# Kernel optimization log

Hardware: AMD Instinct MI355X
Metric: run time of the kernel (lower is better)

## Reference

```python
import jax, jax.numpy as jnp
import numpy as np

B, T, D_IN, D_OUT = 4, 2048, 1024, 1024


def setup_inputs() -> dict:
    key = jax.random.key(0)
    k1, k2, k3, k4 = jax.random.split(key, 4)
    s = 0.02  # keep activations in a sane range
    x = jax.random.normal(k1, (B, T, D_IN), dtype=jnp.float32)
    Wq = jax.random.normal(k2, (D_IN, D_OUT), dtype=jnp.float32) * s
    Wk = jax.random.normal(k3, (D_IN, D_OUT), dtype=jnp.float32) * s
    Wv = jax.random.normal(k4, (D_IN, D_OUT), dtype=jnp.float32) * s
    return {"x": x, "Wq": Wq, "Wk": Wk, "Wv": Wv}


def reference(x, Wq, Wk, Wv):
    # Linear projections (torch Linear: y = x @ W^T, here W stored as [d_in, d_out])
    q = jnp.einsum('btd,de->bte', x, Wq)
    k = jnp.einsum('btd,de,->bte', x, Wk, jnp.float32(1.0)) if False else jnp.einsum('btd,de->bte', x, Wk)
    v = jnp.einsum('btd,de->bte', x, Wv)
    # Full [B, T, T] score matrix (faithful to the hand-rolled implementation)
    scores = jnp.einsum('bqe,bke->bqk', q, k)
    T_ = x.shape[1]
    causal = jnp.triu(jnp.ones((T_, T_), dtype=bool), k=1)  # True above diagonal
    scores = jnp.where(causal[None, :, :], -jnp.inf, scores)
    scale = 1.0 / jnp.sqrt(jnp.asarray(k.shape[-1], dtype=scores.dtype))
    attn = jax.nn.softmax(scores * scale, axis=-1)
    # dropout p=0.0 -> identity
    return jnp.einsum('bqk,bke->bqe', attn, v)
```

## Files before the change

### kernel.cpp

```cpp
#include <hip/hip_runtime.h>
#include <hip/hip_bf16.h>
#include <cstdint>

typedef __attribute__((ext_vector_type(8))) short short8;
typedef __attribute__((ext_vector_type(4))) short short4v;
typedef __attribute__((ext_vector_type(4))) float floatx4;
typedef unsigned short ushort;

__device__ __forceinline__ float bf2f(ushort u) {
  unsigned int x = ((unsigned int)u) << 16;
  return __builtin_bit_cast(float, x);
}
__device__ __forceinline__ ushort f2bf(float f) {
  unsigned int x = __builtin_bit_cast(unsigned int, f);
  x += 0x7fffu + ((x >> 16) & 1u);
  return (ushort)(x >> 16);
}

__device__ __forceinline__ void gload_lds16(const void* g, void* l) {
  __builtin_amdgcn_global_load_lds(
      (const __attribute__((address_space(1))) void*)g,
      (__attribute__((address_space(3))) void*)l, 16, 0, 0);
}


__global__ __launch_bounds__(256) void cvtx_kernel(const float* __restrict__ x,
                                                   ushort* __restrict__ xb) {
  int i = blockIdx.x * 256 + threadIdx.x;
  const float4* xf = (const float4*)x;
  float4 a = xf[i * 2], b = xf[i * 2 + 1];
  short8 o;
  o[0] = (short)f2bf(a.x); o[1] = (short)f2bf(a.y);
  o[2] = (short)f2bf(a.z); o[3] = (short)f2bf(a.w);
  o[4] = (short)f2bf(b.x); o[5] = (short)f2bf(b.y);
  o[6] = (short)f2bf(b.z); o[7] = (short)f2bf(b.w);
  ((short8*)xb)[i] = o;
}

__global__ __launch_bounds__(256) void wt_kernel(const float* __restrict__ Wq,
                                                 const float* __restrict__ Wk,
                                                 const float* __restrict__ Wv,
                                                 ushort* __restrict__ Wt) {
  int z = blockIdx.z;
  const float* W = z == 0 ? Wq : (z == 1 ? Wk : Wv);
  ushort* O = Wt + (size_t)z * 1024 * 1024;
  __shared__ float tile[64][65];
  int c0 = blockIdx.x * 64;
  int r0 = blockIdx.y * 64;
  int tid = threadIdx.x;
#pragma unroll
  for (int i = 0; i < 4; ++i) {
    int c = tid + i * 256; int rr = c >> 4, q = c & 15;
    float4 v = *(const float4*)&W[(size_t)(r0 + rr) * 1024 + c0 + q * 4];
    tile[rr][q * 4 + 0] = v.x; tile[rr][q * 4 + 1] = v.y;
    tile[rr][q * 4 + 2] = v.z; tile[rr][q * 4 + 3] = v.w;
  }
  __syncthreads();
#pragma unroll
  for (int i = 0; i < 2; ++i) {
    int c = tid + i * 256; int oc = c >> 3, q = c & 7;
    short8 o;
#pragma unroll
    for (int j = 0; j < 8; ++j) o[j] = (short)f2bf(tile[q * 8 + j][oc]);
    *(short8*)&O[(size_t)(c0 + oc) * 1024 + r0 + q * 8] = o;
  }
}


__global__ __launch_bounds__(256, 2) void qkv2_kernel(const ushort* __restrict__ A,
                                                      const ushort* __restrict__ Bm,
                                                      ushort* __restrict__ Qo,
                                                      ushort* __restrict__ Ko,
                                                      ushort* __restrict__ Vt) {
  __shared__ __align__(16) ushort ldsA[3][128 * 32];
  __shared__ __align__(16) ushort ldsB[3][256 * 32];

  const int tid = threadIdx.x;
  const int lane = tid & 63;
  const int wave = tid >> 6;
  const int r15 = lane & 15;
  const int kg = lane >> 4;

  int orig = blockIdx.y * 64 + blockIdx.x;
  int swz = (orig & 7) * 96 + (orig >> 3);
  int bx = swz / 12;
  int by = swz % 12;
  const int m0 = bx * 128;
  const int n0 = by * 256;

  const ushort* Ag = A + (size_t)m0 * 1024;
  const ushort* Bg = Bm + (size_t)n0 * 1024;

  const int NKT = 32;

  floatx4 acc[8][4] = {};

  auto stage = [&](int kt, int slot) {
    int k0 = kt * 32;
#pragma unroll
    for (int i = 0; i < 2; ++i) {
      int c = tid + i * 256;
      int d = c * 16;
      int L = d ^ (((d >> 7) & 3) << 4);
      gload_lds16(Ag + (size_t)(L >> 6) * 1024 + k0 + ((L & 63) >> 1),
                  &ldsA[slot][c * 8]);
    }
#pragma unroll
    for (int i = 0; i < 4; ++i) {
      int c = tid + i * 256;
      int d = c * 16;
      int L = d ^ (((d >> 7) & 3) << 4);
      gload_lds16(Bg + (size_t)(L >> 6) * 1024 + k0 + ((L & 63) >> 1),
                  &ldsB[slot][c * 8]);
    }
  };

  auto ldA = [&](int slot, int m) -> short8 {
    int row = m * 16 + r15;
    int P = (row * 64 + kg * 16) ^ (((row >> 1) & 3) << 4);
    return *(const short8*)((const char*)&ldsA[slot][0] + P);
  };
  auto ldB = [&](int slot, int n) -> short8 {
    int row = wave * 64 + n * 16 + r15;
    int P = (row * 64 + kg * 16) ^ (((row >> 1) & 3) << 4);
    return *(const short8*)((const char*)&ldsB[slot][0] + P);
  };

  stage(0, 0);
  stage(1, 1);
  asm volatile("s_waitcnt vmcnt(6)" ::: "memory");
  __builtin_amdgcn_s_barrier();

  int cur = 0;
  for (int kt = 0; kt < NKT; ++kt) {
    short8 bfrag[4], afrag[4];
#pragma unroll
    for (int n = 0; n < 4; ++n) bfrag[n] = ldB(cur, n);
#pragma unroll
    for (int m = 0; m < 4; ++m) afrag[m] = ldA(cur, m);
    if (kt + 2 < NKT) {
      int slot = cur + 2; if (slot >= 3) slot -= 3;
      stage(kt + 2, slot);
    }
    __builtin_amdgcn_s_barrier();
    asm volatile("s_waitcnt lgkmcnt(0)" ::: "memory");
    __builtin_amdgcn_sched_barrier(0);
    __builtin_amdgcn_s_setprio(1);
#pragma unroll
    for (int m = 0; m < 4; ++m)
#pragma unroll
      for (int n = 0; n < 4; ++n)
        acc[m][n] = __builtin_amdgcn_mfma_f32_16x16x32_bf16(afrag[m], bfrag[n], acc[m][n], 0, 0, 0);
    __builtin_amdgcn_s_setprio(0);
    __builtin_amdgcn_s_barrier();

#pragma unroll
    for (int m = 0; m < 4; ++m) afrag[m] = ldA(cur, m + 4);
    if (kt >= NKT - 3) {
      asm volatile("s_waitcnt vmcnt(0)" ::: "memory");
    } else {
      asm volatile("s_waitcnt vmcnt(6)" ::: "memory");
    }
    __builtin_amdgcn_s_barrier();
    asm volatile("s_waitcnt lgkmcnt(0)" ::: "memory");
    __builtin_amdgcn_sched_barrier(0);
    __builtin_amdgcn_s_setprio(1);
#pragma unroll
    for (int m = 0; m < 4; ++m)
#pragma unroll
      for (int n = 0; n < 4; ++n)
        acc[m + 4][n] = __builtin_amdgcn_mfma_f32_16x16x32_bf16(afrag[m], bfrag[n], acc[m + 4][n], 0, 0, 0);
    __builtin_amdgcn_s_setprio(0);
    __builtin_amdgcn_s_barrier();

    ++cur; if (cur >= 3) cur = 0;
  }

  const int z = n0 >> 10;
  const int rq = kg * 4;
  if (z < 2) {
    ushort* Cz = z == 0 ? Qo : Ko;
    const int cb = n0 & 1023;
#pragma unroll
    for (int m = 0; m < 8; ++m) {
#pragma unroll
      for (int n = 0; n < 4; ++n) {
        int gc = cb + wave * 64 + n * 16 + r15;
#pragma unroll
        for (int r = 0; r < 4; ++r) {
          int gr = m0 + m * 16 + rq + r;
          Cz[(size_t)gr * 1024 + gc] = f2bf(acc[m][n][r]);
        }
      }
    }
  } else {
#pragma unroll
    for (int m = 0; m < 8; ++m) {
      int gr = m0 + m * 16 + rq;
      int b = gr >> 11;
      int t = gr & 2047;
      ushort* Vb = Vt + (size_t)b * 1024 * 2048;
#pragma unroll
      for (int n = 0; n < 4; ++n) {
        int e = (n0 - 2048) + wave * 64 + n * 16 + r15;
        short4v o;
#pragma unroll
        for (int r = 0; r < 4; ++r) o[r] = (short)f2bf(acc[m][n][r]);
        *(short4v*)&Vb[(size_t)e * 2048 + t] = o;
      }
    }
  }
}


template <bool OUT_BF16>
__device__ __forceinline__ void gemm_tn_core(const ushort* __restrict__ A,
                                             const ushort* __restrict__ B,
                                             void* __restrict__ C,
                                             int lda, int ldb, int ldc,
                                             int m0, int n0, int kTiles) {
  __shared__ __align__(16) ushort Asm[2][128 * 32];
  __shared__ __align__(16) ushort Bsm[2][128 * 32];
  const int tid = threadIdx.x;
  const int lane = tid & 63;
  const int wave = tid >> 6;
  const int wrow = (wave >> 1) * 64;
  const int wcol = (wave & 1) * 64;
  const int r15 = lane & 15;
  const int kg = (lane >> 4) * 8;

  floatx4 acc[4][4] = {};

  const ushort* Ag = A + (size_t)m0 * lda;
  const ushort* Bg = B + (size_t)n0 * ldb;

  auto stage = [&](int buf, int kt) {
    int k0 = kt * 32;
#pragma unroll
    for (int i = 0; i < 2; ++i) {
      int c = tid + i * 256;
      gload_lds16(Ag + (size_t)(c >> 2) * lda + k0 + (c & 3) * 8, &Asm[buf][c * 8]);
    }
#pragma unroll
    for (int i = 0; i < 2; ++i) {
      int c = tid + i * 256;
      gload_lds16(Bg + (size_t)(c >> 2) * ldb + k0 + (c & 3) * 8, &Bsm[buf][c * 8]);
    }
  };

  stage(0, 0);
  for (int kt = 0; kt < kTiles; ++kt) {
    int cur = kt & 1;
    __syncthreads();
    if (kt + 1 < kTiles) stage(cur ^ 1, kt + 1);
    const ushort* As = Asm[cur];
    const ushort* Bs = Bsm[cur];
    short8 af[4], bfr[4];
#pragma unroll
    for (int m = 0; m < 4; ++m)
      af[m] = *(const short8*)&As[(wrow + m * 16 + r15) * 32 + kg];
#pragma unroll
    for (int n = 0; n < 4; ++n)
      bfr[n] = *(const short8*)&Bs[(wcol + n * 16 + r15) * 32 + kg];
#pragma unroll
    for (int m = 0; m < 4; ++m)
#pragma unroll
      for (int n = 0; n < 4; ++n)
        acc[m][n] = __builtin_amdgcn_mfma_f32_16x16x32_bf16(af[m], bfr[n], acc[m][n], 0, 0, 0);
  }

  const int rq = (lane >> 4) * 4;
#pragma unroll
  for (int m = 0; m < 4; ++m) {
#pragma unroll
    for (int n = 0; n < 4; ++n) {
      int gc = n0 + wcol + n * 16 + r15;
#pragma unroll
      for (int r = 0; r < 4; ++r) {
        int gr = m0 + wrow + m * 16 + rq + r;
        if (OUT_BF16)
          ((ushort*)C)[(size_t)gr * ldc + gc] = f2bf(acc[m][n][r]);
        else
          ((float*)C)[(size_t)gr * ldc + gc] = acc[m][n][r];
      }
    }
  }
}

__global__ __launch_bounds__(256) void s_kernel(const ushort* __restrict__ Q,
                                                const ushort* __restrict__ K,
                                                ushort* __restrict__ S) {
  int t = blockIdx.x;
  int qb = (int)((sqrtf(8.f * (float)t + 1.f) - 1.f) * 0.5f);
  while ((qb + 1) * (qb + 2) / 2 <= t) ++qb;
  while (qb * (qb + 1) / 2 > t) --qb;
  int kb = t - qb * (qb + 1) / 2;
  size_t b = blockIdx.y;
  gemm_tn_core<true>(Q + b * 2048 * 1024, K + b * 2048 * 1024, S + b * 2048 * 2048,
                     1024, 1024, 2048, qb * 128, kb * 128, 32);
}

__global__ __launch_bounds__(256) void pv_kernel(const ushort* __restrict__ P,
                                                 const ushort* __restrict__ Vt,
                                                 float* __restrict__ O) {
  int qb = blockIdx.x;
  size_t b = blockIdx.z;
  gemm_tn_core<false>(P + b * 2048 * 2048, Vt + b * 1024 * 2048, O + b * 2048 * 1024,
                      2048, 2048, 1024, qb * 128, blockIdx.y * 128, (qb + 1) * 4);
}

__global__ __launch_bounds__(256) void softmax_kernel(ushort* __restrict__ S) {
  const int r = blockIdx.x;
  const int b = blockIdx.y;
  ushort* row = S + ((size_t)b * 2048 + r) * 2048;
  const int len = r + 1;
  const int padEnd = ((r >> 7) + 1) << 7;
  const int tid = threadIdx.x;
  const int base = tid * 8;
  const float scale = 0.03125f;

  float v[8];
  float mymax = -1e30f;
  if (base < len) {
    short8 s = *(const short8*)(row + base);
#pragma unroll
    for (int j = 0; j < 8; ++j) {
      float f = (base + j < len) ? bf2f((ushort)s[j]) : -1e30f;
      v[j] = f;
      mymax = fmaxf(mymax, f);
    }
  } else {
#pragma unroll
    for (int j = 0; j < 8; ++j) v[j] = -1e30f;
  }

  __shared__ float redm[4], reds[4];
  const int wave = tid >> 6, lane = tid & 63;
#pragma unroll
  for (int off = 32; off > 0; off >>= 1) mymax = fmaxf(mymax, __shfl_xor(mymax, off, 64));
  if (lane == 0) redm[wave] = mymax;
  __syncthreads();
  float m = fmaxf(fmaxf(redm[0], redm[1]), fmaxf(redm[2], redm[3])) * scale;

  float p[8];
  float mysum = 0.f;
#pragma unroll
  for (int j = 0; j < 8; ++j) {
    float e = (base + j < len) ? __expf(v[j] * scale - m) : 0.f;
    p[j] = e;
    mysum += e;
  }
#pragma unroll
  for (int off = 32; off > 0; off >>= 1) mysum += __shfl_xor(mysum, off, 64);
  if (lane == 0) reds[wave] = mysum;
  __syncthreads();
  float inv = 1.f / (reds[0] + reds[1] + reds[2] + reds[3]);

  if (base < padEnd) {
    short8 o;
#pragma unroll
    for (int j = 0; j < 8; ++j) o[j] = (short)f2bf(p[j] * inv);
    *(short8*)(row + base) = o;
  }
}


extern "C" void kernel_launch(void* const* d_in, const int* in_sizes, int n_in,
                              void* d_out, int out_size, void* d_ws, size_t ws_size,
                              hipStream_t stream) {
  const float* x  = (const float*)d_in[0];
  const float* Wq = (const float*)d_in[1];
  const float* Wk = (const float*)d_in[2];
  const float* Wv = (const float*)d_in[3];
  float* out = (float*)d_out;

  ushort* Xb  = (ushort*)d_ws;
  ushort* Wt  = Xb + (size_t)8192 * 1024;
  ushort* QK  = Wt + (size_t)3 * 1024 * 1024;
  ushort* Vt  = QK + (size_t)2 * 8192 * 1024;
  ushort* S   = Vt + (size_t)4 * 1024 * 2048;

  ushort* Qp = QK;
  ushort* Kp = QK + (size_t)8192 * 1024;

  hipLaunchKernelGGL(cvtx_kernel, dim3(4096), dim3(256), 0, stream, x, Xb);
  hipLaunchKernelGGL(wt_kernel, dim3(16, 16, 3), dim3(256), 0, stream, Wq, Wk, Wv, Wt);
  hipLaunchKernelGGL(qkv2_kernel, dim3(64, 12), dim3(256), 0, stream, Xb, Wt, Qp, Kp, Vt);
  hipLaunchKernelGGL(s_kernel, dim3(136, 4), dim3(256), 0, stream, Qp, Kp, S);
  hipLaunchKernelGGL(softmax_kernel, dim3(2048, 4), dim3(256), 0, stream, S);
  hipLaunchKernelGGL(pv_kernel, dim3(16, 8, 4), dim3(256), 0, stream, S, Vt, out);
}
```

Measured before the change: 187.3 us.

## Enlarge QKV projection GEMM tile to 256x256 with 8 waves and BK=64 staging

The fused QKV projection GEMM moves from a 128x256 tile with 4 waves to a 256x256 tile with 8 waves arranged 2x4, which halves the grid. Each K step now covers 64 columns split into two 32-wide halves, double-buffered in 64KB of LDS. Global-to-LDS loads are issued in quarter-stage chunks interleaved with the four MFMA phases. The goal is more reuse per loaded byte and less global traffic, at the cost of more LDS per block and lower occupancy, which could leave fewer blocks resident per CU.

```diff
diff --git a/kernel.cpp b/kernel.cpp
--- a/kernel.cpp
+++ b/kernel.cpp
@@ -67,114 +67,114 @@
 }
 
 
-__global__ __launch_bounds__(256, 2) void qkv2_kernel(const ushort* __restrict__ A,
+__global__ __launch_bounds__(512, 2) void qkv8_kernel(const ushort* __restrict__ A,
                                                       const ushort* __restrict__ Bm,
                                                       ushort* __restrict__ Qo,
                                                       ushort* __restrict__ Ko,
                                                       ushort* __restrict__ Vt) {
-  __shared__ __align__(16) ushort ldsA[3][128 * 32];
-  __shared__ __align__(16) ushort ldsB[3][256 * 32];
+  __shared__ __align__(16) ushort lds[2][2][2][8192];
 
   const int tid = threadIdx.x;
   const int lane = tid & 63;
   const int wave = tid >> 6;
+  const int wm = wave >> 2;
+  const int wn = wave & 3;
   const int r15 = lane & 15;
   const int kg = lane >> 4;
 
-  int orig = blockIdx.y * 64 + blockIdx.x;
-  int swz = (orig & 7) * 96 + (orig >> 3);
+  int orig = blockIdx.y * 32 + blockIdx.x;
+  int swz = (orig & 7) * 48 + (orig >> 3);
+  int by = swz % 12;
   int bx = swz / 12;
-  int by = swz % 12;
-  const int m0 = bx * 128;
+  const int m0 = bx * 256;
   const int n0 = by * 256;
 
   const ushort* Ag = A + (size_t)m0 * 1024;
   const ushort* Bg = Bm + (size_t)n0 * 1024;
 
-  const int NKT = 32;
+  const int NKT = 16;
 
   floatx4 acc[8][4] = {};
 
-  auto stage = [&](int kt, int slot) {
-    int k0 = kt * 32;
+  auto stage = [&](int j, int h) {
+    const int isA = h & 1;
+    const int kh = h >> 1;
+    ushort* dst = &lds[j & 1][isA ? 0 : 1][kh][0];
+    const ushort* src = isA ? Ag : Bg;
+    const int kbase = j * 64 + kh * 32;
 #pragma unroll
     for (int i = 0; i < 2; ++i) {
-      int c = tid + i * 256;
-      int d = c * 16;
+      int t = tid + i * 512;
+      int d = t * 16;
       int L = d ^ (((d >> 7) & 3) << 4);
-      gload_lds16(Ag + (size_t)(L >> 6) * 1024 + k0 + ((L & 63) >> 1),
-                  &ldsA[slot][c * 8]);
-    }
-#pragma unroll
-    for (int i = 0; i < 4; ++i) {
-      int c = tid + i * 256;
-      int d = c * 16;
-      int L = d ^ (((d >> 7) & 3) << 4);
-      gload_lds16(Bg + (size_t)(L >> 6) * 1024 + k0 + ((L & 63) >> 1),
-                  &ldsB[slot][c * 8]);
+      gload_lds16(src + (size_t)(L >> 6) * 1024 + kbase + ((L & 63) >> 1),
+                  dst + t * 8);
     }
   };
 
-  auto ldA = [&](int slot, int m) -> short8 {
-    int row = m * 16 + r15;
+  auto ldA = [&](int buf, int kh, int m) -> short8 {
+    int row = wm * 128 + m * 16 + r15;
     int P = (row * 64 + kg * 16) ^ (((row >> 1) & 3) << 4);
-    return *(const short8*)((const char*)&ldsA[slot][0] + P);
+    return *(const short8*)((const char*)&lds[buf][0][kh][0] + P);
   };
-  auto ldB = [&](int slot, int n) -> short8 {
-    int row = wave * 64 + n * 16 + r15;
+  auto ldB = [&](int buf, int kh, int n) -> short8 {
+    int row = wn * 64 + n * 16 + r15;
     int P = (row * 64 + kg * 16) ^ (((row >> 1) & 3) << 4);
-    return *(const short8*)((const char*)&ldsB[slot][0] + P);
+    return *(const short8*)((const char*)&lds[buf][1][kh][0] + P);
   };
 
-  stage(0, 0);
-  stage(1, 1);
+#pragma unroll
+  for (int s = 0; s < 7; ++s) stage(s >> 2, s & 3);
   asm volatile("s_waitcnt vmcnt(6)" ::: "memory");
   __builtin_amdgcn_s_barrier();
 
-  int cur = 0;
+#define PHASE_MFMA(MS)                                                              \
+  __builtin_amdgcn_s_barrier();                                                     \
+  asm volatile("s_waitcnt lgkmcnt(0)" ::: "memory");                                \
+  __builtin_amdgcn_sched_barrier(0);                                                \
+  __builtin_amdgcn_s_setprio(1);                                                    \
+  _Pragma("unroll") for (int m = 0; m < 4; ++m)                                     \
+  _Pragma("unroll") for (int n = 0; n < 4; ++n)                                     \
+      acc[(MS) + m][n] = __builtin_amdgcn_mfma_f32_16x16x32_bf16(                   \
+          afrag[m], bfrag[n], acc[(MS) + m][n], 0, 0, 0);                           \
+  __builtin_amdgcn_s_setprio(0);                                                    \
+  __builtin_amdgcn_s_barrier();
+
+  short8 bfrag[4], afrag[4];
   for (int kt = 0; kt < NKT; ++kt) {
-    short8 bfrag[4], afrag[4];
-#pragma unroll
-    for (int n = 0; n < 4; ++n) bfrag[n] = ldB(cur, n);
-#pragma unroll
-    for (int m = 0; m < 4; ++m) afrag[m] = ldA(cur, m);
-    if (kt + 2 < NKT) {
-      int slot = cur + 2; if (slot >= 3) slot -= 3;
-      stage(kt + 2, slot);
-    }
-    __builtin_amdgcn_s_barrier();
-    asm volatile("s_waitcnt lgkmcnt(0)" ::: "memory");
-    __builtin_amdgcn_sched_barrier(0);
-    __builtin_amdgcn_s_setprio(1);
-#pragma unroll
-    for (int m = 0; m < 4; ++m)
-#pragma unroll
-      for (int n = 0; n < 4; ++n)
-        acc[m][n] = __builtin_amdgcn_mfma_f32_16x16x32_bf16(afrag[m], bfrag[n], acc[m][n], 0, 0, 0);
-    __builtin_amdgcn_s_setprio(0);
-    __builtin_amdgcn_s_barrier();
-
-#pragma unroll
-    for (int m = 0; m < 4; ++m) afrag[m] = ldA(cur, m + 4);
-    if (kt >= NKT - 3) {
+    const int buf = kt & 1;
+    const int sb = 7 + kt * 4;
+
+#pragma unroll
+    for (int n = 0; n < 4; ++n) bfrag[n] = ldB(buf, 0, n);
+#pragma unroll
+    for (int m = 0; m < 4; ++m) afrag[m] = ldA(buf, 0, m);
+    if (((sb + 0) >> 2) < NKT) stage((sb + 0) >> 2, (sb + 0) & 3);
+    PHASE_MFMA(0)
+
+#pragma unroll
+    for (int m = 0; m < 4; ++m) afrag[m] = ldA(buf, 0, m + 4);
+    if (((sb + 1) >> 2) < NKT) stage((sb + 1) >> 2, (sb + 1) & 3);
+    PHASE_MFMA(4)
+
+#pragma unroll
+    for (int n = 0; n < 4; ++n) bfrag[n] = ldB(buf, 1, n);
+#pragma unroll
+    for (int m = 0; m < 4; ++m) afrag[m] = ldA(buf, 1, m);
+    if (((sb + 2) >> 2) < NKT) stage((sb + 2) >> 2, (sb + 2) & 3);
+    PHASE_MFMA(0)
+
+#pragma unroll
+    for (int m = 0; m < 4; ++m) afrag[m] = ldA(buf, 1, m + 4);
+    if (((sb + 3) >> 2) < NKT) stage((sb + 3) >> 2, (sb + 3) & 3);
+    if (kt < NKT - 2) {
+      asm volatile("s_waitcnt vmcnt(6)" ::: "memory");
+    } else if (kt == NKT - 2) {
       asm volatile("s_waitcnt vmcnt(0)" ::: "memory");
-    } else {
-      asm volatile("s_waitcnt vmcnt(6)" ::: "memory");
-    }
-    __builtin_amdgcn_s_barrier();
-    asm volatile("s_waitcnt lgkmcnt(0)" ::: "memory");
-    __builtin_amdgcn_sched_barrier(0);
-    __builtin_amdgcn_s_setprio(1);
-#pragma unroll
-    for (int m = 0; m < 4; ++m)
-#pragma unroll
-      for (int n = 0; n < 4; ++n)
-        acc[m + 4][n] = __builtin_amdgcn_mfma_f32_16x16x32_bf16(afrag[m], bfrag[n], acc[m + 4][n], 0, 0, 0);
-    __builtin_amdgcn_s_setprio(0);
-    __builtin_amdgcn_s_barrier();
-
-    ++cur; if (cur >= 3) cur = 0;
-  }
+    }
+    PHASE_MFMA(4)
+  }
+#undef PHASE_MFMA
 
   const int z = n0 >> 10;
   const int rq = kg * 4;
@@ -185,10 +185,10 @@
     for (int m = 0; m < 8; ++m) {
 #pragma unroll
       for (int n = 0; n < 4; ++n) {
-        int gc = cb + wave * 64 + n * 16 + r15;
+        int gc = cb + wn * 64 + n * 16 + r15;
 #pragma unroll
         for (int r = 0; r < 4; ++r) {
-          int gr = m0 + m * 16 + rq + r;
+          int gr = m0 + wm * 128 + m * 16 + rq + r;
           Cz[(size_t)gr * 1024 + gc] = f2bf(acc[m][n][r]);
         }
       }
@@ -196,13 +196,13 @@
   } else {
 #pragma unroll
     for (int m = 0; m < 8; ++m) {
-      int gr = m0 + m * 16 + rq;
+      int gr = m0 + wm * 128 + m * 16 + rq;
       int b = gr >> 11;
       int t = gr & 2047;
       ushort* Vb = Vt + (size_t)b * 1024 * 2048;
 #pragma unroll
       for (int n = 0; n < 4; ++n) {
-        int e = (n0 - 2048) + wave * 64 + n * 16 + r15;
+        int e = (n0 - 2048) + wn * 64 + n * 16 + r15;
         short4v o;
 #pragma unroll
         for (int r = 0; r < 4; ++r) o[r] = (short)f2bf(acc[m][n][r]);
@@ -385,7 +385,7 @@
 
   hipLaunchKernelGGL(cvtx_kernel, dim3(4096), dim3(256), 0, stream, x, Xb);
   hipLaunchKernelGGL(wt_kernel, dim3(16, 16, 3), dim3(256), 0, stream, Wq, Wk, Wv, Wt);
-  hipLaunchKernelGGL(qkv2_kernel, dim3(64, 12), dim3(256), 0, stream, Xb, Wt, Qp, Kp, Vt);
+  hipLaunchKernelGGL(qkv8_kernel, dim3(32, 12), dim3(512), 0, stream, Xb, Wt, Qp, Kp, Vt);
   hipLaunchKernelGGL(s_kernel, dim3(136, 4), dim3(256), 0, stream, Qp, Kp, S);
   hipLaunchKernelGGL(softmax_kernel, dim3(2048, 4), dim3(256), 0, stream, S);
   hipLaunchKernelGGL(pv_kernel, dim3(16, 8, 4), dim3(256), 0, stream, S, Vt, out);
```

Result: no change. 185.3 us (-1.1%).
